# Optimization experiments

Hardware: AMD Instinct MI355X
Metric: run time of the kernel (lower is better)

Reference implementation:

```python
import jax, jax.numpy as jnp
import numpy as np

D_MODEL = 1024
NUM_HEADS = 16
D_K = D_MODEL // NUM_HEADS


def setup_inputs() -> dict:
    key = jax.random.key(0)
    ks = jax.random.split(key, 11)
    s = 1.0 / np.sqrt(D_MODEL)
    return {
        "Q": jax.random.normal(ks[0], (2, 2048, D_MODEL), jnp.float32),
        "K": jax.random.normal(ks[1], (2, 2048, D_MODEL), jnp.float32),
        "V": jax.random.normal(ks[2], (2, 2048, D_MODEL), jnp.float32),
        "W_Q": jax.random.uniform(ks[3], (D_MODEL, D_MODEL), jnp.float32, -s, s),
        "b_Q": jax.random.uniform(ks[4], (D_MODEL,), jnp.float32, -s, s),
        "W_K": jax.random.uniform(ks[5], (D_K, D_MODEL), jnp.float32, -s, s),
        "b_K": jax.random.uniform(ks[6], (D_K,), jnp.float32, -s, s),
        "W_V": jax.random.uniform(ks[7], (D_K, D_MODEL), jnp.float32, -s, s),
        "b_V": jax.random.uniform(ks[8], (D_K,), jnp.float32, -s, s),
        "W_O": jax.random.uniform(ks[9], (D_MODEL, D_MODEL), jnp.float32, -s, s),
        "b_O": jax.random.uniform(ks[10], (D_MODEL,), jnp.float32, -s, s),
    }


def reference(Q, K, V, W_Q, b_Q, W_K, b_K, W_V, b_V, W_O, b_O):
    B, S, _ = Q.shape
    # Q projection -> [B, H, S, d_k]
    q = (Q @ W_Q.T + b_Q).reshape(B, S, NUM_HEADS, D_K).transpose(0, 2, 1, 3)
    # shared single-head K/V -> [B, S, d_k] (broadcast across heads)
    k = K @ W_K.T + b_K
    v = V @ W_V.T + b_V
    scale = 1.0 / jnp.sqrt(jnp.asarray(D_K, q.dtype))
    scores = jnp.einsum('bhqd,bkd->bhqk', q, k) * scale  # [B,H,S,S]
    attn = jax.nn.softmax(scores, axis=-1)
    out = jnp.einsum('bhqk,bkd->bhqd', attn, v)  # [B,H,S,d_k]
    out = out.transpose(0, 2, 1, 3).reshape(B, S, D_MODEL)
    return out @ W_O.T + b_O
```

## Files before the change

### kernel.cpp

```cpp
#include <hip/hip_runtime.h>
#include <hip/hip_bf16.h>
#include <math.h>

#define D_MODEL 1024
#define NUM_HEADS 16
#define DK 64
#define BATCH 2
#define SEQ 2048
#define MROWS (BATCH * SEQ)

#define QSCALE (0.125f * 1.4426950408889634f)

typedef __attribute__((ext_vector_type(8))) short bf16x8;
typedef __attribute__((ext_vector_type(4))) float f32x4;

static __device__ __forceinline__ short f2bf(float f) {
    __hip_bfloat16 h = __float2bfloat16(f);
    union { __hip_bfloat16 h; short s; } c; c.h = h; return c.s;
}

static __device__ __forceinline__ unsigned pkbf2(float a, float b) {
    __hip_bfloat162 h = __float22bfloat162_rn(make_float2(a, b));
    union { __hip_bfloat162 h; unsigned u; } c; c.h = h; return c.u;
}

static __device__ __forceinline__ void gload16(const void* g, void* l) {
    __builtin_amdgcn_global_load_lds(
        (const __attribute__((address_space(1))) unsigned int*)g,
        (__attribute__((address_space(3))) unsigned int*)l, 16, 0, 0);
}

__global__ __launch_bounds__(256) void cvt6(
    const float* __restrict__ q, const float* __restrict__ k,
    const float* __restrict__ v, const float* __restrict__ wq,
    const float* __restrict__ wo, const float* __restrict__ wk,
    const float* __restrict__ wv,
    short* __restrict__ qo, short* __restrict__ ko, short* __restrict__ vo,
    short* __restrict__ wqo, short* __restrict__ woo, short* __restrict__ wko,
    short* __restrict__ wvo)
{
    const int NB = (MROWS * D_MODEL) / 8;
    const int NW = (D_MODEL * D_MODEL) / 8;
    const int NS = (DK * D_MODEL) / 8;
    const int total = 3 * NB + 2 * NW + 2 * NS;
    for (int g = blockIdx.x * 256 + threadIdx.x; g < total; g += gridDim.x * 256) {
        const float* s; short* d; int x = g;
        if (x < NB)            { s = q;  d = qo;  }
        else if ((x -= NB) < NB) { s = k;  d = ko;  }
        else if ((x -= NB) < NB) { s = v;  d = vo;  }
        else if ((x -= NB) < NW) { s = wq; d = wqo; }
        else if ((x -= NW) < NW) { s = wo; d = woo; }
        else if ((x -= NW) < NS) { s = wk; d = wko; }
        else                     { x -= NS; s = wv; d = wvo; }
        float4 a = ((const float4*)s)[x * 2];
        float4 b = ((const float4*)s)[x * 2 + 1];
        uint4 hv;
        hv.x = pkbf2(a.x, a.y); hv.y = pkbf2(a.z, a.w);
        hv.z = pkbf2(b.x, b.y); hv.w = pkbf2(b.z, b.w);
        ((uint4*)d)[x] = hv;
    }
}

template<int MODE, int BM, int BN>
__global__ __launch_bounds__(256) void gemm97(
    const short* __restrict__ A, const short* __restrict__ W,
    const float* __restrict__ bias, void* __restrict__ Cp,
    const short* __restrict__ A2, const short* __restrict__ W2,
    const float* __restrict__ bias2, void* __restrict__ Cp2,
    int M, int N, int K, float outmult)
{
    constexpr int MI = BM / 32;
    constexpr int NI = BN / 32;
    constexpr int ACH = BM / 32;
    constexpr int WCH = BN / 32;
    __shared__ short As[BM * 64];
    __shared__ short Ws[BN * 64];

    int sel = 0;
    if (MODE == 2) {
        sel = blockIdx.y;
        if (sel) { A = A2; W = W2; bias = bias2; Cp = Cp2; }
    }
    const int bm = blockIdx.x * BM;
    const int bn = (MODE == 2) ? 0 : blockIdx.y * BN;
    const int tid = threadIdx.x;
    const int l = tid & 63, w = tid >> 6;
    const int lr = l & 15, lg = l >> 4;
    const int wm = (w >> 1) * (BM / 2), wn = (w & 1) * (BN / 2);

    f32x4 acc[MI][NI];
    #pragma unroll
    for (int mi = 0; mi < MI; mi++)
        #pragma unroll
        for (int ni = 0; ni < NI; ni++)
            acc[mi][ni] = (f32x4){0.f, 0.f, 0.f, 0.f};

    const int srow = l >> 3;
    const int scol = (l & 7) * 8;

    for (int k0 = 0; k0 < K; k0 += 64) {
        __syncthreads();
        #pragma unroll
        for (int i = 0; i < ACH; i++) {
            int c = w * ACH + i;
            gload16(A + (size_t)(bm + 8 * c + srow) * K + k0 + scol, As + c * 512);
        }
        #pragma unroll
        for (int i = 0; i < WCH; i++) {
            int c = w * WCH + i;
            gload16(W + (size_t)(bn + 8 * c + srow) * K + k0 + scol, Ws + c * 512);
        }
        __syncthreads();
        #pragma unroll
        for (int ks = 0; ks < 2; ks++) {
            bf16x8 af[MI], bf[NI];
            #pragma unroll
            for (int mi = 0; mi < MI; mi++)
                af[mi] = *(const bf16x8*)&As[(wm + mi * 16 + lr) * 64 + ks * 32 + 8 * lg];
            #pragma unroll
            for (int ni = 0; ni < NI; ni++)
                bf[ni] = *(const bf16x8*)&Ws[(wn + ni * 16 + lr) * 64 + ks * 32 + 8 * lg];
            #pragma unroll
            for (int mi = 0; mi < MI; mi++)
                #pragma unroll
                for (int ni = 0; ni < NI; ni++)
                    acc[mi][ni] = __builtin_amdgcn_mfma_f32_16x16x32_bf16(
                        af[mi], bf[ni], acc[mi][ni], 0, 0, 0);
        }
    }

    #pragma unroll
    for (int ni = 0; ni < NI; ni++) {
        int col = bn + wn + ni * 16 + lr;
        float bv = bias[col];
        #pragma unroll
        for (int mi = 0; mi < MI; mi++) {
            #pragma unroll
            for (int r = 0; r < 4; r++) {
                int row = bm + wm + mi * 16 + lg * 4 + r;
                float val = (acc[mi][ni][r] + bv) * outmult;
                if (MODE == 0) {
                    ((short*)Cp)[(size_t)row * N + col] = f2bf(val);
                } else if (MODE == 1) {
                    ((float*)Cp)[(size_t)row * N + col] = val;
                } else {
                    if (sel == 0) {
                        ((short*)Cp)[(size_t)row * DK + col] = f2bf(val);
                    } else {
                        int bi = row >> 11, si = row & (SEQ - 1);
                        int s6 = si & 63;
                        int sperm = (si & ~63) | (s6 & 32) |
                                    (((s6 >> 3) & 1) << 4) | (((s6 >> 2) & 1) << 3) |
                                    (((s6 >> 4) & 1) << 2) | (s6 & 3);
                        ((short*)Cp)[((size_t)bi * DK + col) * SEQ + sperm] = f2bf(val);
                    }
                }
            }
        }
    }
}

__global__ __launch_bounds__(256, 4) void mqa_attn_lds(
    const short* __restrict__ qb, const short* __restrict__ kb,
    const short* __restrict__ vt, short* __restrict__ ob)
{
    __shared__ char KsB[2][64 * 128];
    __shared__ char VsB[2][64 * 128];
    const int h = blockIdx.y, b = blockIdx.z;
    const int tid = threadIdx.x;
    const int l = tid & 63, w = tid >> 6;
    const int lr = l & 15, lg = l >> 4;
    const int q0 = blockIdx.x * 64 + w * 16;

    bf16x8 qf[2];
    #pragma unroll
    for (int kk = 0; kk < 2; kk++)
        qf[kk] = *(const bf16x8*)(
            qb + (size_t)(b * SEQ + q0 + lr) * D_MODEL + h * DK + kk * 32 + 8 * lg);

    int srow[2], scol[2];
    #pragma unroll
    for (int i = 0; i < 2; i++) {
        int s = i * 256 + w * 64 + l;
        srow[i] = s >> 3;
        int cb = (s & 7) * 16;
        scol[i] = (cb ^ ((srow[i] & 7) << 4)) >> 1;
    }

    f32x4 o[4];
    #pragma unroll
    for (int dt = 0; dt < 4; dt++)
        o[dt] = (f32x4){0.f, 0.f, 0.f, 0.f};
    float m_i = -1e30f;
    float l_l = 0.f;

    #pragma unroll
    for (int i = 0; i < 2; i++) {
        gload16(kb + (size_t)(b * SEQ + 0 + srow[i]) * DK + scol[i],
                KsB[0] + (i * 256 + w * 64) * 16);
        gload16(vt + (size_t)(b * DK + srow[i]) * SEQ + 0 + scol[i],
                VsB[0] + (i * 256 + w * 64) * 16);
    }

    for (int t = 0; t < SEQ / 64; t++) {
        const int cur = t & 1;
        const int kt = t * 64;
        __syncthreads();
        if (t + 1 < SEQ / 64) {
            const int ktn = kt + 64;
            #pragma unroll
            for (int i = 0; i < 2; i++) {
                gload16(kb + (size_t)(b * SEQ + ktn + srow[i]) * DK + scol[i],
                        KsB[cur ^ 1] + (i * 256 + w * 64) * 16);
                gload16(vt + (size_t)(b * DK + srow[i]) * SEQ + ktn + scol[i],
                        VsB[cur ^ 1] + (i * 256 + w * 64) * 16);
            }
        }
        const char* Kc = KsB[cur];
        const char* Vc = VsB[cur];

        f32x4 s[4];
        #pragma unroll
        for (int j = 0; j < 4; j++) s[j] = (f32x4){0.f, 0.f, 0.f, 0.f};
        #pragma unroll
        for (int kk = 0; kk < 2; kk++) {
            bf16x8 kf[4];
            #pragma unroll
            for (int j = 0; j < 4; j++) {
                int row = j * 16 + lr;
                kf[j] = *(const bf16x8*)(Kc + row * 128 + ((kk * 64 + 16 * lg) ^ ((row & 7) << 4)));
            }
            __builtin_amdgcn_s_setprio(1);
            #pragma unroll
            for (int j = 0; j < 4; j++)
                s[j] = __builtin_amdgcn_mfma_f32_16x16x32_bf16(
                    kf[j], qf[kk], s[j], 0, 0, 0);
            __builtin_amdgcn_s_setprio(0);
        }

        bf16x8 vf[2][4];
        #pragma unroll
        for (int kk = 0; kk < 2; kk++)
            #pragma unroll
            for (int dt = 0; dt < 4; dt++) {
                int row = dt * 16 + lr;
                vf[kk][dt] = *(const bf16x8*)(Vc + row * 128 + ((kk * 64 + 16 * lg) ^ ((row & 7) << 4)));
            }

        union { unsigned u[4]; bf16x8 v; } pku[2];
        {
            float mA = fmaxf(fmaxf(s[0][0], s[0][1]), s[0][2]);
            float mB = fmaxf(fmaxf(s[0][3], s[1][0]), s[1][1]);
            float mC = fmaxf(fmaxf(s[1][2], s[1][3]), s[2][0]);
            float mD = fmaxf(fmaxf(s[2][1], s[2][2]), s[2][3]);
            float mE = fmaxf(fmaxf(s[3][0], s[3][1]), s[3][2]);
            float mx = fmaxf(fmaxf(fmaxf(mA, mB), mC),
                             fmaxf(fmaxf(mD, mE), s[3][3]));

            if (__any(mx > m_i + 8.0f)) {
                float mxf = fmaxf(mx, __shfl_xor(mx, 16));
                mxf = fmaxf(mxf, __shfl_xor(mxf, 32));
                float mn = fmaxf(m_i, mxf);
                float corr = __builtin_amdgcn_exp2f(m_i - mn);
                m_i = mn;
                l_l *= corr;
                #pragma unroll
                for (int dt = 0; dt < 4; dt++)
                    o[dt] *= corr;
            }
            const float mnv = m_i;

            float p[4][4];
            float rs = 0.f;
            #pragma unroll
            for (int j = 0; j < 4; j++) {
                p[j][0] = __builtin_amdgcn_exp2f(s[j][0] - mnv);
                p[j][1] = __builtin_amdgcn_exp2f(s[j][1] - mnv);
                p[j][2] = __builtin_amdgcn_exp2f(s[j][2] - mnv);
                p[j][3] = __builtin_amdgcn_exp2f(s[j][3] - mnv);
                rs += (p[j][0] + p[j][1]) + (p[j][2] + p[j][3]);
            }
            l_l += rs;

            pku[0].u[0] = pkbf2(p[0][0], p[0][1]);
            pku[0].u[1] = pkbf2(p[0][2], p[0][3]);
            pku[0].u[2] = pkbf2(p[1][0], p[1][1]);
            pku[0].u[3] = pkbf2(p[1][2], p[1][3]);
            pku[1].u[0] = pkbf2(p[2][0], p[2][1]);
            pku[1].u[1] = pkbf2(p[2][2], p[2][3]);
            pku[1].u[2] = pkbf2(p[3][0], p[3][1]);
            pku[1].u[3] = pkbf2(p[3][2], p[3][3]);
        }

        __builtin_amdgcn_s_setprio(1);
        #pragma unroll
        for (int kk = 0; kk < 2; kk++)
            #pragma unroll
            for (int dt = 0; dt < 4; dt++)
                o[dt] = __builtin_amdgcn_mfma_f32_16x16x32_bf16(
                    vf[kk][dt], pku[kk].v, o[dt], 0, 0, 0);
        __builtin_amdgcn_s_setprio(0);
    }

    float lt = l_l;
    lt += __shfl_xor(lt, 16);
    lt += __shfl_xor(lt, 32);
    float inv = 1.0f / lt;
    size_t grow = (size_t)(b * SEQ + q0 + lr);
    #pragma unroll
    for (int dt = 0; dt < 4; dt++) {
        uint2 pk;
        pk.x = pkbf2(o[dt][0] * inv, o[dt][1] * inv);
        pk.y = pkbf2(o[dt][2] * inv, o[dt][3] * inv);
        *(uint2*)(ob + grow * D_MODEL + h * DK + dt * 16 + lg * 4) = pk;
    }
}

extern "C" void kernel_launch(void* const* d_in, const int* in_sizes, int n_in,
                              void* d_out, int out_size, void* d_ws, size_t ws_size,
                              hipStream_t stream) {
    const float* Q   = (const float*)d_in[0];
    const float* K   = (const float*)d_in[1];
    const float* V   = (const float*)d_in[2];
    const float* W_Q = (const float*)d_in[3];
    const float* b_Q = (const float*)d_in[4];
    const float* W_K = (const float*)d_in[5];
    const float* b_K = (const float*)d_in[6];
    const float* W_V = (const float*)d_in[7];
    const float* b_V = (const float*)d_in[8];
    const float* W_O = (const float*)d_in[9];
    const float* b_O = (const float*)d_in[10];
    float* out = (float*)d_out;

    short* Qb  = (short*)d_ws;
    short* Kb  = Qb  + (size_t)MROWS * D_MODEL;
    short* Vb  = Kb  + (size_t)MROWS * D_MODEL;
    short* WQb = Vb  + (size_t)MROWS * D_MODEL;
    short* WKb = WQb + (size_t)D_MODEL * D_MODEL;
    short* WVb = WKb + (size_t)DK * D_MODEL;
    short* WOb = WVb + (size_t)DK * D_MODEL;
    short* qb  = WOb + (size_t)D_MODEL * D_MODEL;
    short* kb  = qb  + (size_t)MROWS * D_MODEL;
    short* vt  = kb  + (size_t)MROWS * DK;
    short* aws = vt  + (size_t)MROWS * DK;

    cvt6<<<2048, 256, 0, stream>>>(Q, K, V, W_Q, W_O, W_K, W_V,
                                   Qb, Kb, Vb, WQb, WOb, WKb, WVb);

    gemm97<0, 64, 128><<<dim3(MROWS / 64, D_MODEL / 128), 256, 0, stream>>>(
        Qb, WQb, b_Q, qb, nullptr, nullptr, nullptr, nullptr,
        MROWS, D_MODEL, D_MODEL, QSCALE);
    gemm97<2, 64, 64><<<dim3(MROWS / 64, 2), 256, 0, stream>>>(
        Kb, WKb, b_K, kb, Vb, WVb, b_V, vt, MROWS, DK, D_MODEL, 1.0f);
    mqa_attn_lds<<<dim3(SEQ / 64, NUM_HEADS, BATCH), 256, 0, stream>>>(
        qb, kb, vt, aws);
    gemm97<1, 64, 128><<<dim3(MROWS / 64, D_MODEL / 128), 256, 0, stream>>>(
        aws, WOb, b_O, out, nullptr, nullptr, nullptr, nullptr,
        MROWS, D_MODEL, D_MODEL, 1.0f);
}
```

Baseline: 126.5 us.

## Use 32x32x16 MFMA with split-KV across wave pairs in attention kernel

```diff
diff --git a/kernel.cpp b/kernel.cpp
--- a/kernel.cpp
+++ b/kernel.cpp
@@ -13,6 +13,7 @@
 
 typedef __attribute__((ext_vector_type(8))) short bf16x8;
 typedef __attribute__((ext_vector_type(4))) float f32x4;
+typedef __attribute__((ext_vector_type(16))) float f32x16;
 
 static __device__ __forceinline__ short f2bf(float f) {
     __hip_bfloat16 h = __float2bfloat16(f);
@@ -149,9 +150,10 @@
                     } else {
                         int bi = row >> 11, si = row & (SEQ - 1);
                         int s6 = si & 63;
-                        int sperm = (si & ~63) | (s6 & 32) |
-                                    (((s6 >> 3) & 1) << 4) | (((s6 >> 2) & 1) << 3) |
-                                    (((s6 >> 4) & 1) << 2) | (s6 & 3);
+                        int rr = (s6 & 3) | (((s6 >> 3) & 3) << 2);
+                        int cc = ((s6 >> 5) << 1) | ((rr >> 3) & 1);
+                        int x = cc * 16 + ((s6 >> 2) & 1) * 8 + (rr & 7);
+                        int sperm = (si & ~63) | x;
                         ((short*)Cp)[((size_t)bi * DK + col) * SEQ + sperm] = f2bf(val);
                     }
                 }
@@ -166,42 +168,46 @@
 {
     __shared__ char KsB[2][64 * 128];
     __shared__ char VsB[2][64 * 128];
-    const int h = blockIdx.y, b = blockIdx.z;
+    const int hd = blockIdx.y, b = blockIdx.z;
     const int tid = threadIdx.x;
     const int l = tid & 63, w = tid >> 6;
-    const int lr = l & 15, lg = l >> 4;
-    const int q0 = blockIdx.x * 64 + w * 16;
-
-    bf16x8 qf[2];
-    #pragma unroll
-    for (int kk = 0; kk < 2; kk++)
-        qf[kk] = *(const bf16x8*)(
-            qb + (size_t)(b * SEQ + q0 + lr) * D_MODEL + h * DK + kk * 32 + 8 * lg);
+    const int qg = w >> 1, kh = w & 1;
+    const int lc = l & 31, hh = l >> 5;
+    const int q0 = blockIdx.x * 64 + qg * 32;
+    const int sw = (l & 7) << 4;
+
+    bf16x8 qf[4];
+    #pragma unroll
+    for (int ch = 0; ch < 4; ch++)
+        qf[ch] = *(const bf16x8*)(
+            qb + (size_t)(b * SEQ + q0 + lc) * D_MODEL + hd * DK + ch * 16 + 8 * hh);
 
     int srow[2], scol[2];
     #pragma unroll
     for (int i = 0; i < 2; i++) {
-        int s = i * 256 + w * 64 + l;
+        int s = i * 256 + tid;
         srow[i] = s >> 3;
         int cb = (s & 7) * 16;
         scol[i] = (cb ^ ((srow[i] & 7) << 4)) >> 1;
     }
 
-    f32x4 o[4];
-    #pragma unroll
-    for (int dt = 0; dt < 4; dt++)
-        o[dt] = (f32x4){0.f, 0.f, 0.f, 0.f};
+    f32x16 o[2];
+    #pragma unroll
+    for (int dt = 0; dt < 2; dt++)
+        #pragma unroll
+        for (int i = 0; i < 16; i++) o[dt][i] = 0.f;
     float m_i = -1e30f;
     float l_l = 0.f;
 
     #pragma unroll
     for (int i = 0; i < 2; i++) {
         gload16(kb + (size_t)(b * SEQ + 0 + srow[i]) * DK + scol[i],
-                KsB[0] + (i * 256 + w * 64) * 16);
+                KsB[0] + (i * 256 + tid) * 16);
         gload16(vt + (size_t)(b * DK + srow[i]) * SEQ + 0 + scol[i],
-                VsB[0] + (i * 256 + w * 64) * 16);
-    }
-
+                VsB[0] + (i * 256 + tid) * 16);
+    }
+
+    const int krow = kh * 32 + lc;
     for (int t = 0; t < SEQ / 64; t++) {
         const int cur = t & 1;
         const int kt = t * 64;
@@ -211,108 +217,120 @@
             #pragma unroll
             for (int i = 0; i < 2; i++) {
                 gload16(kb + (size_t)(b * SEQ + ktn + srow[i]) * DK + scol[i],
-                        KsB[cur ^ 1] + (i * 256 + w * 64) * 16);
+                        KsB[cur ^ 1] + (i * 256 + tid) * 16);
                 gload16(vt + (size_t)(b * DK + srow[i]) * SEQ + ktn + scol[i],
-                        VsB[cur ^ 1] + (i * 256 + w * 64) * 16);
+                        VsB[cur ^ 1] + (i * 256 + tid) * 16);
             }
         }
         const char* Kc = KsB[cur];
         const char* Vc = VsB[cur];
 
-        f32x4 s[4];
-        #pragma unroll
-        for (int j = 0; j < 4; j++) s[j] = (f32x4){0.f, 0.f, 0.f, 0.f};
-        #pragma unroll
-        for (int kk = 0; kk < 2; kk++) {
+        f32x16 s;
+        #pragma unroll
+        for (int i = 0; i < 16; i++) s[i] = 0.f;
+        {
+            const char* kbase = Kc + krow * 128;
             bf16x8 kf[4];
             #pragma unroll
-            for (int j = 0; j < 4; j++) {
-                int row = j * 16 + lr;
-                kf[j] = *(const bf16x8*)(Kc + row * 128 + ((kk * 64 + 16 * lg) ^ ((row & 7) << 4)));
-            }
+            for (int ch = 0; ch < 4; ch++)
+                kf[ch] = *(const bf16x8*)(kbase + ((ch * 32 + 16 * hh) ^ sw));
             __builtin_amdgcn_s_setprio(1);
             #pragma unroll
-            for (int j = 0; j < 4; j++)
-                s[j] = __builtin_amdgcn_mfma_f32_16x16x32_bf16(
-                    kf[j], qf[kk], s[j], 0, 0, 0);
+            for (int ch = 0; ch < 4; ch++)
+                s = __builtin_amdgcn_mfma_f32_32x32x16_bf16(kf[ch], qf[ch], s, 0, 0, 0);
             __builtin_amdgcn_s_setprio(0);
         }
 
-        bf16x8 vf[2][4];
-        #pragma unroll
-        for (int kk = 0; kk < 2; kk++)
-            #pragma unroll
-            for (int dt = 0; dt < 4; dt++) {
-                int row = dt * 16 + lr;
-                vf[kk][dt] = *(const bf16x8*)(Vc + row * 128 + ((kk * 64 + 16 * lg) ^ ((row & 7) << 4)));
+        bf16x8 vf[2][2];
+        #pragma unroll
+        for (int dt = 0; dt < 2; dt++)
+            #pragma unroll
+            for (int c2 = 0; c2 < 2; c2++) {
+                int row = dt * 32 + lc;
+                vf[dt][c2] = *(const bf16x8*)(
+                    Vc + row * 128 + ((64 * kh + 32 * c2 + 16 * hh) ^ sw));
             }
 
         union { unsigned u[4]; bf16x8 v; } pku[2];
         {
-            float mA = fmaxf(fmaxf(s[0][0], s[0][1]), s[0][2]);
-            float mB = fmaxf(fmaxf(s[0][3], s[1][0]), s[1][1]);
-            float mC = fmaxf(fmaxf(s[1][2], s[1][3]), s[2][0]);
-            float mD = fmaxf(fmaxf(s[2][1], s[2][2]), s[2][3]);
-            float mE = fmaxf(fmaxf(s[3][0], s[3][1]), s[3][2]);
-            float mx = fmaxf(fmaxf(fmaxf(mA, mB), mC),
-                             fmaxf(fmaxf(mD, mE), s[3][3]));
+            float mA = fmaxf(fmaxf(s[0], s[1]), fmaxf(s[2], s[3]));
+            float mB = fmaxf(fmaxf(s[4], s[5]), fmaxf(s[6], s[7]));
+            float mC = fmaxf(fmaxf(s[8], s[9]), fmaxf(s[10], s[11]));
+            float mD = fmaxf(fmaxf(s[12], s[13]), fmaxf(s[14], s[15]));
+            float mx = fmaxf(fmaxf(mA, mB), fmaxf(mC, mD));
 
             if (__any(mx > m_i + 8.0f)) {
-                float mxf = fmaxf(mx, __shfl_xor(mx, 16));
-                mxf = fmaxf(mxf, __shfl_xor(mxf, 32));
+                float mxf = fmaxf(mx, __shfl_xor(mx, 32));
                 float mn = fmaxf(m_i, mxf);
                 float corr = __builtin_amdgcn_exp2f(m_i - mn);
                 m_i = mn;
                 l_l *= corr;
+                o[0] *= corr;
+                o[1] *= corr;
+            }
+            const float mnv = m_i;
+            float rs = 0.f;
+            #pragma unroll
+            for (int c2 = 0; c2 < 2; c2++)
                 #pragma unroll
-                for (int dt = 0; dt < 4; dt++)
-                    o[dt] *= corr;
-            }
-            const float mnv = m_i;
-
-            float p[4][4];
-            float rs = 0.f;
-            #pragma unroll
-            for (int j = 0; j < 4; j++) {
-                p[j][0] = __builtin_amdgcn_exp2f(s[j][0] - mnv);
-                p[j][1] = __builtin_amdgcn_exp2f(s[j][1] - mnv);
-                p[j][2] = __builtin_amdgcn_exp2f(s[j][2] - mnv);
-                p[j][3] = __builtin_amdgcn_exp2f(s[j][3] - mnv);
-                rs += (p[j][0] + p[j][1]) + (p[j][2] + p[j][3]);
-            }
+                for (int i = 0; i < 4; i++) {
+                    float p0 = __builtin_amdgcn_exp2f(s[8 * c2 + 2 * i] - mnv);
+                    float p1 = __builtin_amdgcn_exp2f(s[8 * c2 + 2 * i + 1] - mnv);
+                    rs += p0 + p1;
+                    pku[c2].u[i] = pkbf2(p0, p1);
+                }
             l_l += rs;
-
-            pku[0].u[0] = pkbf2(p[0][0], p[0][1]);
-            pku[0].u[1] = pkbf2(p[0][2], p[0][3]);
-            pku[0].u[2] = pkbf2(p[1][0], p[1][1]);
-            pku[0].u[3] = pkbf2(p[1][2], p[1][3]);
-            pku[1].u[0] = pkbf2(p[2][0], p[2][1]);
-            pku[1].u[1] = pkbf2(p[2][2], p[2][3]);
-            pku[1].u[2] = pkbf2(p[3][0], p[3][1]);
-            pku[1].u[3] = pkbf2(p[3][2], p[3][3]);
         }
 
         __builtin_amdgcn_s_setprio(1);
         #pragma unroll
-        for (int kk = 0; kk < 2; kk++)
-            #pragma unroll
-            for (int dt = 0; dt < 4; dt++)
-                o[dt] = __builtin_amdgcn_mfma_f32_16x16x32_bf16(
-                    vf[kk][dt], pku[kk].v, o[dt], 0, 0, 0);
+        for (int c2 = 0; c2 < 2; c2++)
+            #pragma unroll
+            for (int dt = 0; dt < 2; dt++)
+                o[dt] = __builtin_amdgcn_mfma_f32_32x32x16_bf16(
+                    vf[dt][c2], pku[c2].v, o[dt], 0, 0, 0);
         __builtin_amdgcn_s_setprio(0);
     }
 
-    float lt = l_l;
-    lt += __shfl_xor(lt, 16);
-    lt += __shfl_xor(lt, 32);
-    float inv = 1.0f / lt;
-    size_t grow = (size_t)(b * SEQ + q0 + lr);
-    #pragma unroll
-    for (int dt = 0; dt < 4; dt++) {
-        uint2 pk;
-        pk.x = pkbf2(o[dt][0] * inv, o[dt][1] * inv);
-        pk.y = pkbf2(o[dt][2] * inv, o[dt][3] * inv);
-        *(uint2*)(ob + grow * D_MODEL + h * DK + dt * 16 + lg * 4) = pk;
+    float lw = l_l + __shfl_xor(l_l, 32);
+    __syncthreads();
+    float* ML = (float*)VsB;
+    char* OB = (char*)KsB;
+    if (kh == 1) {
+        if (l < 32) { ML[qg * 64 + l] = m_i; ML[qg * 64 + 32 + l] = lw; }
+        char* myO = OB + ((size_t)qg * 64 + l) * 128;
+        #pragma unroll
+        for (int dt = 0; dt < 2; dt++)
+            #pragma unroll
+            for (int i = 0; i < 4; i++) {
+                f32x4 vv = { o[dt][4 * i], o[dt][4 * i + 1],
+                             o[dt][4 * i + 2], o[dt][4 * i + 3] };
+                *(f32x4*)(myO + (((dt * 4 + i) * 16) ^ sw)) = vv;
+            }
+    }
+    __syncthreads();
+    if (kh == 0) {
+        float m1 = ML[qg * 64 + lc];
+        float l1 = ML[qg * 64 + 32 + lc];
+        float mM = fmaxf(m_i, m1);
+        float c0 = __builtin_amdgcn_exp2f(m_i - mM);
+        float c1 = __builtin_amdgcn_exp2f(m1 - mM);
+        float inv = 1.0f / (lw * c0 + l1 * c1);
+        float a0 = c0 * inv, a1 = c1 * inv;
+        const char* oO = OB + ((size_t)qg * 64 + l) * 128;
+        size_t grow = (size_t)(b * SEQ + q0 + lc);
+        #pragma unroll
+        for (int dt = 0; dt < 2; dt++)
+            #pragma unroll
+            for (int rq = 0; rq < 4; rq++) {
+                f32x4 ov = *(const f32x4*)(oO + (((dt * 4 + rq) * 16) ^ sw));
+                uint2 pk;
+                pk.x = pkbf2(o[dt][4 * rq]     * a0 + ov[0] * a1,
+                             o[dt][4 * rq + 1] * a0 + ov[1] * a1);
+                pk.y = pkbf2(o[dt][4 * rq + 2] * a0 + ov[2] * a1,
+                             o[dt][4 * rq + 3] * a0 + ov[3] * a1);
+                *(uint2*)(ob + grow * D_MODEL + hd * DK + dt * 32 + rq * 8 + 4 * hh) = pk;
+            }
     }
 }
 
```

New measurement: 167.2 us. +32.2%, slower.
